# Performance work log

Hardware: AMD Instinct MI355X
Metric: run time of the kernel (lower is better)

Reference implementation:

```python
import jax, jax.numpy as jnp
import numpy as np

# Static sizes (RED-GNN on ICEWS14-like graph)
B = 32          # batch (queries)
N = 100000      # active nodes per layer (fixed frontier size)
E = 1000000     # edges per layer
H = 64          # hidden_dim
A = 5           # attn_dim
L = 3           # n_layer
N_REL = 230
N_ENT = 7128
N_TIME = 365


def setup_inputs() -> dict:
    key = jax.random.key(0)
    ks = jax.random.split(key, 16)
    inp = {}
    # edge structure (constant w.r.t. differentiation)
    inp['batch_idx'] = jax.random.randint(ks[0], (E,), 0, B)
    inp['src_idx'] = jax.random.randint(ks[1], (E,), 0, N)
    inp['dst_idx'] = jax.random.randint(ks[2], (E,), 0, N)
    inp['rel_idx'] = jax.random.randint(ks[3], (E,), 0, N_REL + 1)
    # signed relative time in [-(N_TIME-1), N_TIME-1]
    inp['rel_time'] = jax.random.randint(ks[4], (E,), -(N_TIME - 1), N_TIME)
    inp['query_rel'] = jax.random.randint(ks[5], (B,), 0, N_REL + 1)
    # unique (batch, entity) slot per final node
    n = jnp.arange(N)
    inp['out_batch'] = n // N_ENT
    inp['out_ent'] = n % N_ENT
    # learned parameters
    s = 1.0 / np.sqrt(H)
    inp['rela_embed'] = jax.random.normal(ks[6], (L, N_REL + 1, H), jnp.float32) * s
    inp['time_embed'] = jax.random.normal(ks[7], (N_TIME, H), jnp.float32) * s
    inp['Wp'] = jax.random.normal(ks[8], (H, H), jnp.float32) * s
    inp['Wn'] = jax.random.normal(ks[9], (H, H), jnp.float32) * s
    inp['Wf'] = jax.random.normal(ks[10], (H, H), jnp.float32) * s
    inp['W1'] = jax.random.normal(ks[11], (L, A, 3 * H), jnp.float32) * s
    inp['W2'] = jax.random.normal(ks[12], (L, 1, A), jnp.float32) / np.sqrt(A)
    inp['Wc'] = jax.random.normal(ks[13], (1, H), jnp.float32) * s
    inp['bc'] = jnp.zeros((1,), jnp.float32)
    return inp


def reference(rela_embed, time_embed, Wp, Wn, Wf, W1, W2, Wc, bc,
              batch_idx, src_idx, dst_idx, rel_idx, rel_time,
              query_rel, out_batch, out_ent):
    hidden = jnp.zeros((N, H), dtype=rela_embed.dtype)
    q_rel_e = query_rel[batch_idx]                 # [E]
    t_emb = time_embed[jnp.abs(rel_time)]          # [E,H]
    pos = (rel_time > 0)[:, None]
    zer = (rel_time == 0)[:, None]
    for i in range(L):
        rel_e = rela_embed[i][rel_idx]             # [E,H]
        embed = hidden[src_idx] + rel_e + t_emb    # [E,H]
        # branch by sign of relative time: future / now / past linear
        transformed = jnp.where(pos, embed @ Wf.T,
                      jnp.where(zer, embed @ Wn.T, embed @ Wp.T))
        attn_in = jnp.concatenate(
            [hidden[src_idx], rel_e, rela_embed[i][q_rel_e]], axis=1)  # [E,3H]
        score = jax.nn.sigmoid(
            jax.nn.relu(attn_in @ W1[i].T) @ W2[i].T)  # [E,1]
        msg = score * transformed                      # [E,H]
        hidden = jax.nn.relu(
            jax.ops.segment_sum(msg, dst_idx, num_segments=N))
    result = (hidden @ Wc.T + bc).reshape(-1)          # [N]
    score_all = jnp.zeros((B, N_ENT), result.dtype)
    score_all = score_all.at[out_batch, out_ent].set(result)
    return score_all
```

## Files before the change

### kernel.cpp

```cpp
#include <hip/hip_runtime.h>

#define NB   32
#define NN   100000
#define NE   1000000
#define HD   64
#define AD   5
#define NL   3
#define NRL  231
#define NTM  365
#define NOUT 228096
#define NBLK1 391
#define BLKN 32
#define NBLK2 3125


__device__ __forceinline__ float bflo(unsigned u) { return __uint_as_float(u << 16); }
__device__ __forceinline__ float bfhi(unsigned u) { return __uint_as_float(u & 0xffff0000u); }
__device__ __forceinline__ unsigned packbf2(float x, float y) {
    unsigned ux = __float_as_uint(x), uy = __float_as_uint(y);
    ux = (ux + 0x7fffu + ((ux >> 16) & 1u)) >> 16;
    uy = (uy + 0x7fffu + ((uy >> 16) & 1u)) >> 16;
    return ux | (uy << 16);
}

using vbf8  = __attribute__((ext_vector_type(8))) short;
using f32x4 = __attribute__((ext_vector_type(4))) float;

__global__ __launch_bounds__(256) void prep_wtb_kernel(
    const float* __restrict__ Wp, const float* __restrict__ Wn,
    const float* __restrict__ Wf, ushort* __restrict__ WTB)
{
    int i = blockIdx.x * 256 + threadIdx.x;
    if (i >= 3072) return;
    int lane = i & 63;
    int nt = (i >> 6) & 3;
    int ks = (i >> 8) & 1;
    int hl = (i >> 9) & 1;
    int c  = i >> 10;
    const float* W = (c == 0) ? Wf : (c == 1 ? Wn : Wp);
    int h  = nt * 16 + (lane & 15);
    int k0 = ks * 32 + (lane >> 4) * 8;
    unsigned up[4];
    #pragma unroll
    for (int j = 0; j < 4; ++j) {
        float x = W[h * 64 + k0 + 2 * j];
        float y = W[h * 64 + k0 + 2 * j + 1];
        unsigned pb = packbf2(x, y);
        if (hl) {
            float rx = x - bflo(pb);
            float ry = y - bfhi(pb);
            pb = packbf2(rx, ry);
        }
        up[j] = pb;
    }
    *(uint4*)(WTB + (size_t)i * 8) = make_uint4(up[0], up[1], up[2], up[3]);
}

__global__ __launch_bounds__(256) void prep_tb_kernel(
    const float* __restrict__ rela_embed,
    const float* __restrict__ time_embed,
    ushort* __restrict__ relb,
    ushort* __restrict__ tembb)
{
    const int nrel_w = 3 * NRL * HD / 2;
    const int ntmb_w = NTM * HD / 2;
    int i = blockIdx.x * 256 + threadIdx.x;
    if (i < nrel_w) {
        ((unsigned*)relb)[i] = packbf2(rela_embed[2 * i], rela_embed[2 * i + 1]);
    } else if (i < nrel_w + ntmb_w) {
        int k = i - nrel_w;
        ((unsigned*)tembb)[k] = packbf2(time_embed[2 * k], time_embed[2 * k + 1]);
    }
}

__global__ __launch_bounds__(256) void prep_tables_kernel(
    const float* __restrict__ rela_embed,
    const float* __restrict__ W1,
    float* __restrict__ Trel,
    float* __restrict__ Tq)
{
    int l = blockIdx.x;
    int r = threadIdx.x;
    if (r >= NRL) return;
    const float4* rrow = (const float4*)(rela_embed + ((size_t)l * NRL + r) * HD);
    const float* W1l = W1 + (size_t)l * AD * 192;
    float tr[AD] = {0,0,0,0,0}, tq[AD] = {0,0,0,0,0};
    #pragma unroll
    for (int k4 = 0; k4 < 16; ++k4) {
        float4 x = rrow[k4];
        #pragma unroll
        for (int a = 0; a < AD; ++a) {
            const float* wr = W1l + a * 192 + 64 + k4 * 4;
            const float* wq = W1l + a * 192 + 128 + k4 * 4;
            tr[a] = fmaf(x.x, wr[0], tr[a]); tr[a] = fmaf(x.y, wr[1], tr[a]);
            tr[a] = fmaf(x.z, wr[2], tr[a]); tr[a] = fmaf(x.w, wr[3], tr[a]);
            tq[a] = fmaf(x.x, wq[0], tq[a]); tq[a] = fmaf(x.y, wq[1], tq[a]);
            tq[a] = fmaf(x.z, wq[2], tq[a]); tq[a] = fmaf(x.w, wq[3], tq[a]);
        }
    }
    float* tro = Trel + ((size_t)l * NRL + r) * 8;
    float* tqo = Tq   + ((size_t)l * NRL + r) * 8;
    #pragma unroll
    for (int a = 0; a < AD; ++a) { tro[a] = tr[a]; tqo[a] = tq[a]; }
    tro[5] = tro[6] = tro[7] = 0.f;
    tqo[5] = tqo[6] = tqo[7] = 0.f;
}

__global__ __launch_bounds__(256) void hist_kernel(
    const int* __restrict__ dst_idx, int* __restrict__ deg,
    ushort* __restrict__ rank)
{
    int e = blockIdx.x * 256 + threadIdx.x;
    if (e < NE) rank[e] = (ushort)atomicAdd(&deg[dst_idx[e]], 1);
}

__global__ __launch_bounds__(256) void scan1_kernel(
    const int* __restrict__ deg, int* __restrict__ tmp, int* __restrict__ bsum)
{
    __shared__ int s[256];
    int tid = threadIdx.x;
    int i = blockIdx.x * 256 + tid;
    int v = (i < NN) ? deg[i] : 0;
    s[tid] = v;
    __syncthreads();
    #pragma unroll
    for (int st = 1; st < 256; st <<= 1) {
        int t = (tid >= st) ? s[tid - st] : 0;
        __syncthreads();
        s[tid] += t;
        __syncthreads();
    }
    if (i < NN) tmp[i] = s[tid];
    if (tid == 255) bsum[blockIdx.x] = s[255];
}

__global__ __launch_bounds__(512) void scan2_kernel(
    const int* __restrict__ bsum, int* __restrict__ bpref)
{
    __shared__ int s[512];
    int tid = threadIdx.x;
    int v = (tid < NBLK1) ? bsum[tid] : 0;
    s[tid] = v;
    __syncthreads();
    #pragma unroll
    for (int st = 1; st < 512; st <<= 1) {
        int t = (tid >= st) ? s[tid - st] : 0;
        __syncthreads();
        s[tid] += t;
        __syncthreads();
    }
    if (tid < NBLK1) bpref[tid] = s[tid] - v;
}

__global__ __launch_bounds__(256) void scan3_kernel(
    const int* __restrict__ deg, const int* __restrict__ tmp,
    const int* __restrict__ bpref, int* __restrict__ off)
{
    int i = blockIdx.x * 256 + threadIdx.x;
    if (i >= NN) return;
    int incl = tmp[i] + bpref[i >> 8];
    off[i + 1] = incl;
    if (i == 0) off[0] = 0;
}

__global__ __launch_bounds__(256) void sort_scatter_kernel(
    const int* __restrict__ dst_idx, const int* __restrict__ src_idx,
    const int* __restrict__ rel_idx, const int* __restrict__ rel_time,
    const int* __restrict__ batch_idx, const int* __restrict__ query_rel,
    const int* __restrict__ off, const ushort* __restrict__ rank,
    const float* __restrict__ Trel0, const float* __restrict__ Tq0,
    const float* __restrict__ W2,
    int2* __restrict__ meta, float* __restrict__ score0)
{
    int e = blockIdx.x * 256 + threadIdx.x;
    if (e >= NE) return;
    int d = dst_idx[e];
    int rt = rel_time[e];
    int cls = (rt > 0) ? 0 : ((rt == 0) ? 1 : 2);
    int ta = (rt < 0) ? -rt : rt;
    int rel = rel_idx[e];
    int q = query_rel[batch_idx[e]];
    int pos = off[d] + (int)rank[e];
    int2 m;
    m.x = src_idx[e] | (rel << 17) | (cls << 25);
    m.y = ta | (q << 9);
    meta[pos] = m;

    float4 t0 = *(const float4*)(Trel0 + rel * 8);
    float  t4 = Trel0[rel * 8 + 4];
    float4 u0 = *(const float4*)(Tq0 + q * 8);
    float  u4 = Tq0[q * 8 + 4];
    float z = 0.f;
    z = fmaf(fmaxf(t0.x + u0.x, 0.f), W2[0], z);
    z = fmaf(fmaxf(t0.y + u0.y, 0.f), W2[1], z);
    z = fmaf(fmaxf(t0.z + u0.z, 0.f), W2[2], z);
    z = fmaf(fmaxf(t0.w + u0.w, 0.f), W2[3], z);
    z = fmaf(fmaxf(t4   + u4,   0.f), W2[4], z);
    score0[pos] = 1.f / (1.f + __expf(-z));
}

__global__ __launch_bounds__(256) void score_kernel(
    const float* __restrict__ proj,
    const float* __restrict__ Trel,
    const float* __restrict__ Tq,
    const float* __restrict__ W2,
    const int2* __restrict__ meta,
    float* __restrict__ score)
{
    int j = blockIdx.x * 256 + threadIdx.x;
    if (j >= NE) return;
    int2 mt = meta[j];
    int rel = (mt.x >> 17) & 0xFF;
    int q   = (mt.y >> 9) & 0xFF;
    int src = mt.x & 0x1FFFF;

    float4 t0 = *(const float4*)(Trel + rel * 8);
    float  t4 = Trel[rel * 8 + 4];
    float4 u0 = *(const float4*)(Tq + q * 8);
    float  u4 = Tq[q * 8 + 4];
    float4 p0 = *(const float4*)(proj + (size_t)src * 8);
    float  p4 = proj[(size_t)src * 8 + 4];
    float z = 0.f;
    z = fmaf(fmaxf(p0.x + t0.x + u0.x, 0.f), W2[0], z);
    z = fmaf(fmaxf(p0.y + t0.y + u0.y, 0.f), W2[1], z);
    z = fmaf(fmaxf(p0.z + t0.z + u0.z, 0.f), W2[2], z);
    z = fmaf(fmaxf(p0.w + t0.w + u0.w, 0.f), W2[3], z);
    z = fmaf(fmaxf(p4   + t4   + u4,   0.f), W2[4], z);
    score[j] = 1.f / (1.f + __expf(-z));
}

template <bool HZ>
__device__ __forceinline__ void edge_acc(
    int mx, float sc, uint4 rv, uint4 tv, uint4 hv, float4* __restrict__ A)
{
    int cl = (mx >> 25) & 3;
    float4 v0, v1;
    v0.x = bflo(rv.x) + bflo(tv.x); v0.y = bfhi(rv.x) + bfhi(tv.x);
    v0.z = bflo(rv.y) + bflo(tv.y); v0.w = bfhi(rv.y) + bfhi(tv.y);
    v1.x = bflo(rv.z) + bflo(tv.z); v1.y = bfhi(rv.z) + bfhi(tv.z);
    v1.z = bflo(rv.w) + bflo(tv.w); v1.w = bfhi(rv.w) + bfhi(tv.w);
    if (!HZ) {
        v0.x += bflo(hv.x); v0.y += bfhi(hv.x);
        v0.z += bflo(hv.y); v0.w += bfhi(hv.y);
        v1.x += bflo(hv.z); v1.y += bfhi(hv.z);
        v1.z += bflo(hv.w); v1.w += bfhi(hv.w);
    }
    float sA = (cl == 0) ? sc : 0.f;
    float sB = (cl == 1) ? sc : 0.f;
    float sC = (cl == 2) ? sc : 0.f;
    A[0].x = fmaf(sA, v0.x, A[0].x); A[0].y = fmaf(sA, v0.y, A[0].y);
    A[0].z = fmaf(sA, v0.z, A[0].z); A[0].w = fmaf(sA, v0.w, A[0].w);
    A[1].x = fmaf(sA, v1.x, A[1].x); A[1].y = fmaf(sA, v1.y, A[1].y);
    A[1].z = fmaf(sA, v1.z, A[1].z); A[1].w = fmaf(sA, v1.w, A[1].w);
    A[2].x = fmaf(sB, v0.x, A[2].x); A[2].y = fmaf(sB, v0.y, A[2].y);
    A[2].z = fmaf(sB, v0.z, A[2].z); A[2].w = fmaf(sB, v0.w, A[2].w);
    A[3].x = fmaf(sB, v1.x, A[3].x); A[3].y = fmaf(sB, v1.y, A[3].y);
    A[3].z = fmaf(sB, v1.z, A[3].z); A[3].w = fmaf(sB, v1.w, A[3].w);
    A[4].x = fmaf(sC, v0.x, A[4].x); A[4].y = fmaf(sC, v0.y, A[4].y);
    A[4].z = fmaf(sC, v0.z, A[4].z); A[4].w = fmaf(sC, v0.w, A[4].w);
    A[5].x = fmaf(sC, v1.x, A[5].x); A[5].y = fmaf(sC, v1.y, A[5].y);
    A[5].z = fmaf(sC, v1.z, A[5].z); A[5].w = fmaf(sC, v1.w, A[5].w);
}

__device__ __forceinline__ uint4 ldrow(const ushort* __restrict__ base, int row, int hc8)
{
    return *(const uint4*)(base + (size_t)row * HD + hc8);
}

#define SPITCH 68
template <bool HZ, bool PROJ, bool OUT>
__global__ __launch_bounds__(256, 4) void reduce_transform_kernel(
    const ushort* __restrict__ hidden_in,
    const ushort* __restrict__ relb,
    const ushort* __restrict__ tembb,
    const float* __restrict__ score,
    const int2* __restrict__ meta,
    const int*  __restrict__ off,
    const ushort* __restrict__ WTB,
    const float* __restrict__ W1next,
    ushort* __restrict__ hidden_out,
    float* __restrict__ proj_out,
    const float* __restrict__ Wc,
    const float* __restrict__ bc,
    float* __restrict__ outv)
{
    __shared__ float lds_t[BLKN * SPITCH];
    int tid  = threadIdx.x;
    int lane = tid & 63;
    int w    = __builtin_amdgcn_readfirstlane(tid >> 6);
    int gid  = tid >> 3;
    int hc   = tid & 7;
    int hc8  = hc * 8;
    int node0 = blockIdx.x * BLKN;
    int node  = node0 + gid;

    float4 a[6];
    #pragma unroll
    for (int c = 0; c < 6; ++c)
        a[c] = make_float4(0.f, 0.f, 0.f, 0.f);

    {
        int o0 = off[node];
        int o1 = off[node + 1];
        int j = o0;
        const uint4 zz = make_uint4(0, 0, 0, 0);
        for (; j + 4 <= o1; j += 4) {
            int2 m0 = meta[j],     m1 = meta[j + 1];
            int2 m2 = meta[j + 2], m3 = meta[j + 3];
            float s0 = score[j],     s1 = score[j + 1];
            float s2 = score[j + 2], s3 = score[j + 3];
            uint4 r0 = ldrow(relb, (m0.x >> 17) & 0xFF, hc8);
            uint4 r1 = ldrow(relb, (m1.x >> 17) & 0xFF, hc8);
            uint4 r2 = ldrow(relb, (m2.x >> 17) & 0xFF, hc8);
            uint4 r3 = ldrow(relb, (m3.x >> 17) & 0xFF, hc8);
            uint4 t0 = ldrow(tembb, m0.y & 511, hc8);
            uint4 t1 = ldrow(tembb, m1.y & 511, hc8);
            uint4 t2 = ldrow(tembb, m2.y & 511, hc8);
            uint4 t3 = ldrow(tembb, m3.y & 511, hc8);
            uint4 h0 = zz, h1 = zz, h2 = zz, h3 = zz;
            if (!HZ) {
                h0 = ldrow(hidden_in, m0.x & 0x1FFFF, hc8);
                h1 = ldrow(hidden_in, m1.x & 0x1FFFF, hc8);
                h2 = ldrow(hidden_in, m2.x & 0x1FFFF, hc8);
                h3 = ldrow(hidden_in, m3.x & 0x1FFFF, hc8);
            }
            edge_acc<HZ>(m0.x, s0, r0, t0, h0, a);
            edge_acc<HZ>(m1.x, s1, r1, t1, h1, a);
            edge_acc<HZ>(m2.x, s2, r2, t2, h2, a);
            edge_acc<HZ>(m3.x, s3, r3, t3, h3, a);
        }
        for (; j < o1; ++j) {
            int2 m0 = meta[j];
            float s0 = score[j];
            uint4 r0 = ldrow(relb, (m0.x >> 17) & 0xFF, hc8);
            uint4 t0 = ldrow(tembb, m0.y & 511, hc8);
            uint4 h0 = zz;
            if (!HZ) h0 = ldrow(hidden_in, m0.x & 0x1FFFF, hc8);
            edge_acc<HZ>(m0.x, s0, r0, t0, h0, a);
        }
    }

    unsigned* lds_u = (unsigned*)lds_t;
    int rl = lane & 15;
    int t  = lane >> 4;
    int rt = w & 1;
    int ct = w >> 1;
    f32x4 accd[2];
    accd[0] = (f32x4){0.f, 0.f, 0.f, 0.f};
    accd[1] = (f32x4){0.f, 0.f, 0.f, 0.f};

    #pragma unroll
    for (int c = 0; c < 3; ++c) {
        __syncthreads();
        {
            float4 v0 = a[2 * c];
            float4 v1 = a[2 * c + 1];
            unsigned p0 = packbf2(v0.x, v0.y);
            unsigned p1 = packbf2(v0.z, v0.w);
            unsigned p2 = packbf2(v1.x, v1.y);
            unsigned p3 = packbf2(v1.z, v1.w);
            unsigned q0 = packbf2(v0.x - bflo(p0), v0.y - bfhi(p0));
            unsigned q1 = packbf2(v0.z - bflo(p1), v0.w - bfhi(p1));
            unsigned q2 = packbf2(v1.x - bflo(p2), v1.y - bfhi(p2));
            unsigned q3 = packbf2(v1.z - bflo(p3), v1.w - bfhi(p3));
            *(uint4*)(lds_u + gid * SPITCH + hc * 4)      = make_uint4(p0, p1, p2, p3);
            *(uint4*)(lds_u + gid * SPITCH + 32 + hc * 4) = make_uint4(q0, q1, q2, q3);
        }
        __syncthreads();
        #pragma unroll
        for (int ks = 0; ks < 2; ++ks) {
            const unsigned* rowp = lds_u + (rt * 16 + rl) * SPITCH + ks * 16 + t * 4;
            vbf8 ah = *(const vbf8*)rowp;
            vbf8 al = *(const vbf8*)(rowp + 32);
            #pragma unroll
            for (int b = 0; b < 2; ++b) {
                int nt = ct * 2 + b;
                const ushort* bp = WTB +
                    (size_t)((((c * 2) * 2 + ks) * 4 + nt) * 64 + lane) * 8;
                vbf8 bh = *(const vbf8*)bp;
                vbf8 bl = *(const vbf8*)(bp + 4096);
                accd[b] = __builtin_amdgcn_mfma_f32_16x16x32_bf16(ah, bh, accd[b], 0, 0, 0);
                accd[b] = __builtin_amdgcn_mfma_f32_16x16x32_bf16(al, bh, accd[b], 0, 0, 0);
                accd[b] = __builtin_amdgcn_mfma_f32_16x16x32_bf16(ah, bl, accd[b], 0, 0, 0);
            }
        }
    }

    __syncthreads();
    #pragma unroll
    for (int b = 0; b < 2; ++b)
        #pragma unroll
        for (int i = 0; i < 4; ++i)
            lds_t[(rt * 16 + t * 4 + i) * SPITCH + (ct * 2 + b) * 16 + rl] = accd[b][i];
    __syncthreads();

    float acc8[8];
    {
        const float4* rp = (const float4*)(lds_t + gid * SPITCH + hc8);
        float4 x = rp[0], y = rp[1];
        acc8[0] = x.x; acc8[1] = x.y; acc8[2] = x.z; acc8[3] = x.w;
        acc8[4] = y.x; acc8[5] = y.y; acc8[6] = y.z; acc8[7] = y.w;
    }

    if (!OUT) {
        ushort* outp = hidden_out + (size_t)node * 64 + hc8;
        unsigned u0 = packbf2(fmaxf(acc8[0], 0.f), fmaxf(acc8[1], 0.f));
        unsigned u1 = packbf2(fmaxf(acc8[2], 0.f), fmaxf(acc8[3], 0.f));
        unsigned u2 = packbf2(fmaxf(acc8[4], 0.f), fmaxf(acc8[5], 0.f));
        unsigned u3 = packbf2(fmaxf(acc8[6], 0.f), fmaxf(acc8[7], 0.f));
        *(uint4*)outp = make_uint4(u0, u1, u2, u3);
    }

    if (PROJ) {
        float pa[AD];
        #pragma unroll
        for (int aa = 0; aa < AD; ++aa) pa[aa] = 0.f;
        #pragma unroll
        for (int i = 0; i < 8; ++i) {
            float hv = fmaxf(acc8[i], 0.f);
            #pragma unroll
            for (int aa = 0; aa < AD; ++aa)
                pa[aa] = fmaf(hv, W1next[aa * 192 + hc8 + i], pa[aa]);
        }
        __syncthreads();
        float* lds2 = lds_t;
        #pragma unroll
        for (int aa = 0; aa < AD; ++aa)
            lds2[tid * AD + aa] = pa[aa];
        __syncthreads();
        int nd = tid >> 3, aa = tid & 7;
        float v = 0.f;
        if (aa < AD) {
            #pragma unroll
            for (int ho = 0; ho < 8; ++ho)
                v += lds2[(nd * 8 + ho) * AD + aa];
        }
        proj_out[(size_t)(node0 + nd) * 8 + aa] = v;
    }

    if (OUT) {
        float po = 0.f;
        #pragma unroll
        for (int i = 0; i < 8; ++i)
            po = fmaf(fmaxf(acc8[i], 0.f), Wc[hc8 + i], po);
        po += __shfl_xor(po, 1);
        po += __shfl_xor(po, 2);
        po += __shfl_xor(po, 4);
        if (hc == 0) outv[node] = po + bc[0];
    }
}

extern "C" void kernel_launch(void* const* d_in, const int* in_sizes, int n_in,
                              void* d_out, int out_size, void* d_ws, size_t ws_size,
                              hipStream_t stream)
{
    const int*   batch_idx  = (const int*)d_in[0];
    const int*   src_idx    = (const int*)d_in[1];
    const int*   dst_idx    = (const int*)d_in[2];
    const int*   rel_idx    = (const int*)d_in[3];
    const int*   rel_time   = (const int*)d_in[4];
    const int*   query_rel  = (const int*)d_in[5];
    const float* rela_embed = (const float*)d_in[8];
    const float* time_embed = (const float*)d_in[9];
    const float* Wp         = (const float*)d_in[10];
    const float* Wn         = (const float*)d_in[11];
    const float* Wf         = (const float*)d_in[12];
    const float* W1         = (const float*)d_in[13];
    const float* W2         = (const float*)d_in[14];
    const float* Wc         = (const float*)d_in[15];
    const float* bc         = (const float*)d_in[16];
    float* out = (float*)d_out;

    char* ws = (char*)d_ws;
    ushort* hid0  = (ushort*)(ws + 0);
    ushort* hid1  = (ushort*)(ws + 12800000);
    float* projA  = (float*)(ws + 25600000);
    float* projB  = (float*)(ws + 28800000);
    float* score  = (float*)(ws + 32000000);
    ushort* WTB   = (ushort*)(ws + 36000000);
    float* Trel   = (float*)(ws + 36100000);
    float* Tq     = (float*)(ws + 36130000);
    int*   off    = (int*)  (ws + 36160000);
    int2*  meta   = (int2*) (ws + 37400000);
    int*   deg    = (int*)  (ws + 45400000);
    ushort* relb  = (ushort*)(ws + 45800000);
    ushort* tembb = (ushort*)(ws + 45950000);
    int*   tmp    = (int*)  (ws + 46600000);
    ushort* rank  = (ushort*)(ws + 47000000);
    int*   bsum   = (int*)  (ws + 49000000);
    int*   bpref  = (int*)  (ws + 49010000);

    prep_wtb_kernel<<<12, 256, 0, stream>>>(Wp, Wn, Wf, WTB);
    prep_tb_kernel<<<133, 256, 0, stream>>>(rela_embed, time_embed, relb, tembb);
    prep_tables_kernel<<<NL, 256, 0, stream>>>(rela_embed, W1, Trel, Tq);

    hipMemsetAsync(deg, 0, NN * sizeof(int), stream);
    hipMemsetAsync(out, 0, NOUT * sizeof(float), stream);
    hist_kernel<<<(NE + 255) / 256, 256, 0, stream>>>(dst_idx, deg, rank);
    scan1_kernel<<<NBLK1, 256, 0, stream>>>(deg, tmp, bsum);
    scan2_kernel<<<1, 512, 0, stream>>>(bsum, bpref);
    scan3_kernel<<<NBLK1, 256, 0, stream>>>(deg, tmp, bpref, off);
    sort_scatter_kernel<<<(NE + 255) / 256, 256, 0, stream>>>(
        dst_idx, src_idx, rel_idx, rel_time, batch_idx, query_rel,
        off, rank, Trel, Tq, W2, meta, score);

    int grid = NBLK2;
    int sgrid = (NE + 255) / 256;
    {
        reduce_transform_kernel<true, true, false><<<grid, 256, 0, stream>>>(
            hid1, relb, tembb, score, meta, off,
            WTB, W1 + (size_t)1 * AD * 192, hid0, projA,
            nullptr, nullptr, nullptr);
    }
    {
        score_kernel<<<sgrid, 256, 0, stream>>>(
            projA, Trel + (size_t)1 * NRL * 8, Tq + (size_t)1 * NRL * 8,
            W2 + 1 * AD, meta, score);
        reduce_transform_kernel<false, true, false><<<grid, 256, 0, stream>>>(
            hid0, relb + (size_t)1 * NRL * HD, tembb, score, meta, off,
            WTB, W1 + (size_t)2 * AD * 192, hid1, projB,
            nullptr, nullptr, nullptr);
    }
    {
        score_kernel<<<sgrid, 256, 0, stream>>>(
            projB, Trel + (size_t)2 * NRL * 8, Tq + (size_t)2 * NRL * 8,
            W2 + 2 * AD, meta, score);
        reduce_transform_kernel<false, false, true><<<grid, 256, 0, stream>>>(
            hid1, relb + (size_t)2 * NRL * HD, tembb, score, meta, off,
            WTB, nullptr, nullptr, nullptr,
            Wc, bc, out);
    }
}
```

Measured before the change: 382.8 us.

## Sort edges by time-class within each destination to cut per-edge FMAs

The histogram now counts edges per (destination, time-sign class), and the scan emits per-class base offsets, so edges within each destination segment are grouped by class. The reduce loop keeps a single running partial sum and flushes it into the matching class accumulator only when the class changes. Per-edge work drops from 24 masked FMAs to 8. The cost is a branch per edge, a 3x larger degree array, and extra scan reads. Workspace buffers are rearranged to overlap with the projection buffers, which appears safe because deg2, cbase, tmp and rank are only used before the projection buffers are written.

```diff
diff --git a/kernel.cpp b/kernel.cpp
--- a/kernel.cpp
+++ b/kernel.cpp
@@ -106,21 +106,26 @@
     tqo[5] = tqo[6] = tqo[7] = 0.f;
 }
 
-__global__ __launch_bounds__(256) void hist_kernel(
-    const int* __restrict__ dst_idx, int* __restrict__ deg,
-    ushort* __restrict__ rank)
+__global__ __launch_bounds__(256) void hist2_kernel(
+    const int* __restrict__ dst_idx, const int* __restrict__ rel_time,
+    int* __restrict__ deg2, ushort* __restrict__ rank)
 {
     int e = blockIdx.x * 256 + threadIdx.x;
-    if (e < NE) rank[e] = (ushort)atomicAdd(&deg[dst_idx[e]], 1);
+    if (e < NE) {
+        int d = dst_idx[e];
+        int rt = rel_time[e];
+        int cls = (rt > 0) ? 0 : ((rt == 0) ? 1 : 2);
+        rank[e] = (ushort)atomicAdd(&deg2[d * 3 + cls], 1);
+    }
 }
 
 __global__ __launch_bounds__(256) void scan1_kernel(
-    const int* __restrict__ deg, int* __restrict__ tmp, int* __restrict__ bsum)
+    const int* __restrict__ deg2, int* __restrict__ tmp, int* __restrict__ bsum)
 {
     __shared__ int s[256];
     int tid = threadIdx.x;
     int i = blockIdx.x * 256 + tid;
-    int v = (i < NN) ? deg[i] : 0;
+    int v = (i < NN) ? (deg2[3 * i] + deg2[3 * i + 1] + deg2[3 * i + 2]) : 0;
     s[tid] = v;
     __syncthreads();
     #pragma unroll
@@ -153,13 +158,19 @@
 }
 
 __global__ __launch_bounds__(256) void scan3_kernel(
-    const int* __restrict__ deg, const int* __restrict__ tmp,
-    const int* __restrict__ bpref, int* __restrict__ off)
+    const int* __restrict__ deg2, const int* __restrict__ tmp,
+    const int* __restrict__ bpref, int* __restrict__ off,
+    int* __restrict__ cbase)
 {
     int i = blockIdx.x * 256 + threadIdx.x;
     if (i >= NN) return;
     int incl = tmp[i] + bpref[i >> 8];
+    int d0 = deg2[3 * i], d1 = deg2[3 * i + 1], d2 = deg2[3 * i + 2];
+    int start = incl - (d0 + d1 + d2);
     off[i + 1] = incl;
+    cbase[3 * i]     = start;
+    cbase[3 * i + 1] = start + d0;
+    cbase[3 * i + 2] = start + d0 + d1;
     if (i == 0) off[0] = 0;
 }
 
@@ -167,7 +178,7 @@
     const int* __restrict__ dst_idx, const int* __restrict__ src_idx,
     const int* __restrict__ rel_idx, const int* __restrict__ rel_time,
     const int* __restrict__ batch_idx, const int* __restrict__ query_rel,
-    const int* __restrict__ off, const ushort* __restrict__ rank,
+    const int* __restrict__ cbase, const ushort* __restrict__ rank,
     const float* __restrict__ Trel0, const float* __restrict__ Tq0,
     const float* __restrict__ W2,
     int2* __restrict__ meta, float* __restrict__ score0)
@@ -180,7 +191,7 @@
     int ta = (rt < 0) ? -rt : rt;
     int rel = rel_idx[e];
     int q = query_rel[batch_idx[e]];
-    int pos = off[d] + (int)rank[e];
+    int pos = cbase[d * 3 + cls] + (int)rank[e];
     int2 m;
     m.x = src_idx[e] | (rel << 17) | (cls << 25);
     m.y = ta | (q << 9);
@@ -229,11 +240,37 @@
     score[j] = 1.f / (1.f + __expf(-z));
 }
 
+__device__ __forceinline__ uint4 ldrow(const ushort* __restrict__ base, int row, int hc8)
+{
+    return *(const uint4*)(base + (size_t)row * HD + hc8);
+}
+
+__device__ __forceinline__ void flushp(int cc, float4 p0, float4 p1, float4* __restrict__ A)
+{
+    if (cc == 0) {
+        A[0].x += p0.x; A[0].y += p0.y; A[0].z += p0.z; A[0].w += p0.w;
+        A[1].x += p1.x; A[1].y += p1.y; A[1].z += p1.z; A[1].w += p1.w;
+    } else if (cc == 1) {
+        A[2].x += p0.x; A[2].y += p0.y; A[2].z += p0.z; A[2].w += p0.w;
+        A[3].x += p1.x; A[3].y += p1.y; A[3].z += p1.z; A[3].w += p1.w;
+    } else {
+        A[4].x += p0.x; A[4].y += p0.y; A[4].z += p0.z; A[4].w += p0.w;
+        A[5].x += p1.x; A[5].y += p1.y; A[5].z += p1.z; A[5].w += p1.w;
+    }
+}
+
 template <bool HZ>
-__device__ __forceinline__ void edge_acc(
-    int mx, float sc, uint4 rv, uint4 tv, uint4 hv, float4* __restrict__ A)
-{
-    int cl = (mx >> 25) & 3;
+__device__ __forceinline__ void edge_step(
+    int mx, float sc, uint4 rv, uint4 tv, uint4 hv,
+    int& cc, float4& p0, float4& p1, float4* __restrict__ A)
+{
+    int cls = (mx >> 25) & 3;
+    if (cls != cc) {
+        flushp(cc, p0, p1, A);
+        p0 = make_float4(0.f, 0.f, 0.f, 0.f);
+        p1 = make_float4(0.f, 0.f, 0.f, 0.f);
+        cc = cls;
+    }
     float4 v0, v1;
     v0.x = bflo(rv.x) + bflo(tv.x); v0.y = bfhi(rv.x) + bfhi(tv.x);
     v0.z = bflo(rv.y) + bflo(tv.y); v0.w = bfhi(rv.y) + bfhi(tv.y);
@@ -245,26 +282,10 @@
         v1.x += bflo(hv.z); v1.y += bfhi(hv.z);
         v1.z += bflo(hv.w); v1.w += bfhi(hv.w);
     }
-    float sA = (cl == 0) ? sc : 0.f;
-    float sB = (cl == 1) ? sc : 0.f;
-    float sC = (cl == 2) ? sc : 0.f;
-    A[0].x = fmaf(sA, v0.x, A[0].x); A[0].y = fmaf(sA, v0.y, A[0].y);
-    A[0].z = fmaf(sA, v0.z, A[0].z); A[0].w = fmaf(sA, v0.w, A[0].w);
-    A[1].x = fmaf(sA, v1.x, A[1].x); A[1].y = fmaf(sA, v1.y, A[1].y);
-    A[1].z = fmaf(sA, v1.z, A[1].z); A[1].w = fmaf(sA, v1.w, A[1].w);
-    A[2].x = fmaf(sB, v0.x, A[2].x); A[2].y = fmaf(sB, v0.y, A[2].y);
-    A[2].z = fmaf(sB, v0.z, A[2].z); A[2].w = fmaf(sB, v0.w, A[2].w);
-    A[3].x = fmaf(sB, v1.x, A[3].x); A[3].y = fmaf(sB, v1.y, A[3].y);
-    A[3].z = fmaf(sB, v1.z, A[3].z); A[3].w = fmaf(sB, v1.w, A[3].w);
-    A[4].x = fmaf(sC, v0.x, A[4].x); A[4].y = fmaf(sC, v0.y, A[4].y);
-    A[4].z = fmaf(sC, v0.z, A[4].z); A[4].w = fmaf(sC, v0.w, A[4].w);
-    A[5].x = fmaf(sC, v1.x, A[5].x); A[5].y = fmaf(sC, v1.y, A[5].y);
-    A[5].z = fmaf(sC, v1.z, A[5].z); A[5].w = fmaf(sC, v1.w, A[5].w);
-}
-
-__device__ __forceinline__ uint4 ldrow(const ushort* __restrict__ base, int row, int hc8)
-{
-    return *(const uint4*)(base + (size_t)row * HD + hc8);
+    p0.x = fmaf(sc, v0.x, p0.x); p0.y = fmaf(sc, v0.y, p0.y);
+    p0.z = fmaf(sc, v0.z, p0.z); p0.w = fmaf(sc, v0.w, p0.w);
+    p1.x = fmaf(sc, v1.x, p1.x); p1.y = fmaf(sc, v1.y, p1.y);
+    p1.z = fmaf(sc, v1.z, p1.z); p1.w = fmaf(sc, v1.w, p1.w);
 }
 
 #define SPITCH 68
@@ -303,6 +324,9 @@
         int o0 = off[node];
         int o1 = off[node + 1];
         int j = o0;
+        int cc = 0;
+        float4 p0 = make_float4(0.f, 0.f, 0.f, 0.f);
+        float4 p1 = make_float4(0.f, 0.f, 0.f, 0.f);
         const uint4 zz = make_uint4(0, 0, 0, 0);
         for (; j + 4 <= o1; j += 4) {
             int2 m0 = meta[j],     m1 = meta[j + 1];
@@ -324,10 +348,10 @@
                 h2 = ldrow(hidden_in, m2.x & 0x1FFFF, hc8);
                 h3 = ldrow(hidden_in, m3.x & 0x1FFFF, hc8);
             }
-            edge_acc<HZ>(m0.x, s0, r0, t0, h0, a);
-            edge_acc<HZ>(m1.x, s1, r1, t1, h1, a);
-            edge_acc<HZ>(m2.x, s2, r2, t2, h2, a);
-            edge_acc<HZ>(m3.x, s3, r3, t3, h3, a);
+            edge_step<HZ>(m0.x, s0, r0, t0, h0, cc, p0, p1, a);
+            edge_step<HZ>(m1.x, s1, r1, t1, h1, cc, p0, p1, a);
+            edge_step<HZ>(m2.x, s2, r2, t2, h2, cc, p0, p1, a);
+            edge_step<HZ>(m3.x, s3, r3, t3, h3, cc, p0, p1, a);
         }
         for (; j < o1; ++j) {
             int2 m0 = meta[j];
@@ -336,8 +360,9 @@
             uint4 t0 = ldrow(tembb, m0.y & 511, hc8);
             uint4 h0 = zz;
             if (!HZ) h0 = ldrow(hidden_in, m0.x & 0x1FFFF, hc8);
-            edge_acc<HZ>(m0.x, s0, r0, t0, h0, a);
-        }
+            edge_step<HZ>(m0.x, s0, r0, t0, h0, cc, p0, p1, a);
+        }
+        flushp(cc, p0, p1, a);
     }
 
     unsigned* lds_u = (unsigned*)lds_t;
@@ -474,6 +499,10 @@
     char* ws = (char*)d_ws;
     ushort* hid0  = (ushort*)(ws + 0);
     ushort* hid1  = (ushort*)(ws + 12800000);
+    int*   deg2   = (int*)  (ws + 25600000);
+    int*   cbase  = (int*)  (ws + 26800000);
+    int*   tmp    = (int*)  (ws + 28000000);
+    ushort* rank  = (ushort*)(ws + 28400000);
     float* projA  = (float*)(ws + 25600000);
     float* projB  = (float*)(ws + 28800000);
     float* score  = (float*)(ws + 32000000);
@@ -481,12 +510,9 @@
     float* Trel   = (float*)(ws + 36100000);
     float* Tq     = (float*)(ws + 36130000);
     int*   off    = (int*)  (ws + 36160000);
+    ushort* relb  = (ushort*)(ws + 36600000);
+    ushort* tembb = (ushort*)(ws + 36700000);
     int2*  meta   = (int2*) (ws + 37400000);
-    int*   deg    = (int*)  (ws + 45400000);
-    ushort* relb  = (ushort*)(ws + 45800000);
-    ushort* tembb = (ushort*)(ws + 45950000);
-    int*   tmp    = (int*)  (ws + 46600000);
-    ushort* rank  = (ushort*)(ws + 47000000);
     int*   bsum   = (int*)  (ws + 49000000);
     int*   bpref  = (int*)  (ws + 49010000);
 
@@ -494,15 +520,15 @@
     prep_tb_kernel<<<133, 256, 0, stream>>>(rela_embed, time_embed, relb, tembb);
     prep_tables_kernel<<<NL, 256, 0, stream>>>(rela_embed, W1, Trel, Tq);
 
-    hipMemsetAsync(deg, 0, NN * sizeof(int), stream);
+    hipMemsetAsync(deg2, 0, 3 * NN * sizeof(int), stream);
     hipMemsetAsync(out, 0, NOUT * sizeof(float), stream);
-    hist_kernel<<<(NE + 255) / 256, 256, 0, stream>>>(dst_idx, deg, rank);
-    scan1_kernel<<<NBLK1, 256, 0, stream>>>(deg, tmp, bsum);
+    hist2_kernel<<<(NE + 255) / 256, 256, 0, stream>>>(dst_idx, rel_time, deg2, rank);
+    scan1_kernel<<<NBLK1, 256, 0, stream>>>(deg2, tmp, bsum);
     scan2_kernel<<<1, 512, 0, stream>>>(bsum, bpref);
-    scan3_kernel<<<NBLK1, 256, 0, stream>>>(deg, tmp, bpref, off);
+    scan3_kernel<<<NBLK1, 256, 0, stream>>>(deg2, tmp, bpref, off, cbase);
     sort_scatter_kernel<<<(NE + 255) / 256, 256, 0, stream>>>(
         dst_idx, src_idx, rel_idx, rel_time, batch_idx, query_rel,
-        off, rank, Trel, Tq, W2, meta, score);
+        cbase, rank, Trel, Tq, W2, meta, score);
 
     int grid = NBLK2;
     int sgrid = (NE + 255) / 256;
```

Result: slower. 424.5 us (+10.9%).
